# Kernel optimization log

Measured on AMD Instinct MI355X. Metric: run time of the kernel, lower is better.

Reference implementation:

```python
import jax, jax.numpy as jnp
import numpy as np

N_NODES = 50000
N_EDGES = 500000
N_FEAT = 128
EMB_DIM = 1024
HIDDEN = 128
OUT_DIM = 10
VOCAB = 55049
N_GRAPHS = 64


def setup_inputs() -> dict:
    key = jax.random.key(0)
    ks = jax.random.split(key, 12)
    x = jax.random.normal(ks[0], (N_NODES, N_FEAT), dtype=jnp.float32)
    edge_weight = jax.random.uniform(ks[1], (N_EDGES,), dtype=jnp.float32)
    edge_index = jax.random.randint(ks[2], (2, N_EDGES), 0, N_NODES)
    batch = jnp.sort(jax.random.randint(ks[3], (N_NODES,), 0, N_GRAPHS))
    node_ids = jax.random.randint(ks[4], (N_NODES,), 0, VOCAB)
    emb_table = jax.random.normal(ks[5], (VOCAB, EMB_DIM), dtype=jnp.float32)
    d_in = N_FEAT + EMB_DIM
    W1 = jax.random.normal(ks[6], (d_in, HIDDEN), dtype=jnp.float32) / np.sqrt(d_in)
    b1 = jnp.zeros((HIDDEN,), dtype=jnp.float32)
    W2 = jax.random.normal(ks[7], (HIDDEN, HIDDEN), dtype=jnp.float32) / np.sqrt(HIDDEN)
    b2 = jnp.zeros((HIDDEN,), dtype=jnp.float32)
    fcW = jax.random.normal(ks[8], (HIDDEN, OUT_DIM), dtype=jnp.float32) / np.sqrt(HIDDEN)
    fcb = jnp.zeros((OUT_DIM,), dtype=jnp.float32)
    return dict(x=x, edge_weight=edge_weight, emb_table=emb_table, W1=W1, b1=b1,
                W2=W2, b2=b2, fcW=fcW, fcb=fcb,
                edge_index=edge_index, batch=batch, node_ids=node_ids)


def gcn_conv(x, edge_index, edge_weight, W, b, n_nodes):
    # PyG GCNConv: x' = D^{-1/2} (A + I) D^{-1/2} (x W) + b, self-loop weight = 1
    x = x @ W
    src, dst = edge_index[0], edge_index[1]
    loop = jnp.arange(n_nodes)
    src = jnp.concatenate([src, loop])
    dst = jnp.concatenate([dst, loop])
    ew = jnp.concatenate([edge_weight, jnp.ones((n_nodes,), x.dtype)])
    deg = jax.ops.segment_sum(ew, dst, num_segments=n_nodes)
    dinv = jnp.where(deg > 0, jax.lax.rsqrt(deg), 0.0)
    norm = dinv[src] * ew * dinv[dst]  # [E+N]
    msgs = norm[:, None] * x[src]      # [E+N, H] gather
    out = jax.ops.segment_sum(msgs, dst, num_segments=n_nodes)  # scatter-add
    return out + b


def reference(x, edge_weight, emb_table, W1, b1, W2, b2, fcW, fcb,
              edge_index, batch, node_ids):
    n = x.shape[0]
    h = jnp.concatenate([x, emb_table[node_ids]], axis=1)  # [N, F+E]
    h = jax.nn.relu(gcn_conv(h, edge_index, edge_weight, W1, b1, n))
    h = jax.nn.relu(gcn_conv(h, edge_index, edge_weight, W2, b2, n))
    # global mean pool per graph (dropout is identity in eval)
    sums = jax.ops.segment_sum(h, batch, num_segments=N_GRAPHS)
    counts = jax.ops.segment_sum(jnp.ones((n,), h.dtype), batch, num_segments=N_GRAPHS)
    pooled = sums / jnp.maximum(counts, 1.0)[:, None]
    return pooled @ fcW + fcb
```

## Files before the change

### kernel.cpp

```cpp
#include <hip/hip_runtime.h>
#include <hip/hip_bf16.h>

#define N_NODES 50000
#define N_EDGES 500000
#define N_FEAT 128
#define EMB_DIM 1024
#define HIDDEN 128
#define OUT_DIM 10
#define N_GRAPHS 64
#define NB_NODE 196

typedef __attribute__((ext_vector_type(8))) short short8;
typedef __attribute__((ext_vector_type(4))) float f32x4;

__device__ __forceinline__ unsigned short f2bf(float f) {
    unsigned int u = __float_as_uint(f);
    return (unsigned short)((u + 0x7fffu + ((u >> 16) & 1u)) >> 16);
}
__device__ __forceinline__ float bflo(unsigned int r) { return __uint_as_float(r << 16); }
__device__ __forceinline__ float bfhi(unsigned int r) { return __uint_as_float(r & 0xffff0000u); }
__device__ __forceinline__ unsigned int packbf(float lo, float hi) {
    return ((unsigned int)f2bf(hi) << 16) | f2bf(lo);
}

__global__ __launch_bounds__(256) void k_init(unsigned long long* __restrict__ dc,
                                              float* __restrict__ sums,
                                              float* __restrict__ counts) {
    int i = blockIdx.x * 256 + threadIdx.x;
    if (i < N_NODES) dc[i] = 0ULL;
    if (i < N_GRAPHS * HIDDEN) sums[i] = 0.0f;
    if (i < N_GRAPHS) counts[i] = 0.0f;
}

__global__ __launch_bounds__(256) void k_deg(const int* __restrict__ dst,
                                             const float* __restrict__ ew,
                                             unsigned long long* __restrict__ dc) {
    int e = blockIdx.x * 256 + threadIdx.x;
    if (e < N_EDGES) {
        unsigned int fx = (unsigned int)(ew[e] * 16777216.0f);
        atomicAdd(&dc[dst[e]], (1ULL << 32) | (unsigned long long)fx);
    }
}

__global__ __launch_bounds__(256) void k_scan1(const unsigned long long* __restrict__ dc,
                                               int* __restrict__ bsum) {
    __shared__ int wsum[4];
    int i = blockIdx.x * 256 + threadIdx.x;
    int v = (i < N_NODES) ? (int)((const uint2*)dc)[i].y : 0;
#pragma unroll
    for (int off = 32; off; off >>= 1) v += __shfl_down(v, off, 64);
    if ((threadIdx.x & 63) == 0) wsum[threadIdx.x >> 6] = v;
    __syncthreads();
    if (threadIdx.x == 0) bsum[blockIdx.x] = wsum[0] + wsum[1] + wsum[2] + wsum[3];
}

__global__ __launch_bounds__(256) void k_scan2(int* __restrict__ bsum) {
    __shared__ int sh[256];
    int t = threadIdx.x;
    int v = (t < NB_NODE) ? bsum[t] : 0;
    sh[t] = v;
    __syncthreads();
    for (int off = 1; off < 256; off <<= 1) {
        int add = (t >= off) ? sh[t - off] : 0;
        __syncthreads();
        sh[t] += add;
        __syncthreads();
    }
    if (t < NB_NODE) bsum[t] = sh[t] - v;
}

__global__ __launch_bounds__(256) void k_scan3(const unsigned long long* __restrict__ dc,
                                               const int* __restrict__ bofs,
                                               int* __restrict__ cursor,
                                               int* __restrict__ rowptr,
                                               float* __restrict__ dinv) {
    __shared__ int sh[256];
    const int t = threadIdx.x;
    const int i = blockIdx.x * 256 + t;
    uint2 d = (i < N_NODES) ? ((const uint2*)dc)[i] : make_uint2(0u, 0u);
    int v = (int)d.y;
    sh[t] = v;
    __syncthreads();
    for (int off = 1; off < 256; off <<= 1) {
        int add = (t >= off) ? sh[t - off] : 0;
        __syncthreads();
        sh[t] += add;
        __syncthreads();
    }
    int ex = sh[t] - v + bofs[blockIdx.x];
    if (i < N_NODES) {
        rowptr[i] = ex;
        cursor[i] = ex;
        float deg = 1.0f + (float)d.x * (1.0f / 16777216.0f);
        dinv[i] = 1.0f / sqrtf(deg);
    }
    if (i == 0) rowptr[N_NODES] = N_EDGES;
}

__global__ __launch_bounds__(256) void k_fill(const int* __restrict__ src,
                                              const int* __restrict__ dst,
                                              const float* __restrict__ ew,
                                              const float* __restrict__ dinv,
                                              int* __restrict__ cursor,
                                              int2* __restrict__ csr) {
    int e = blockIdx.x * 256 + threadIdx.x;
    if (e >= N_EDGES) return;
    int s = src[e], d = dst[e];
    int pos = atomicAdd(&cursor[d], 1);
    float norm = dinv[s] * ew[e] * dinv[d];
    csr[pos] = make_int2(s, __float_as_int(norm));
}

__device__ __forceinline__ void prep_one(const float* __restrict__ W,
                                         unsigned short* __restrict__ Wt,
                                         int K, int t) {
    int n = t & 127;
    int c = t >> 7;
    if (c * 16 >= K) return;
    short8 h0, h1;
#pragma unroll
    for (int i = 0; i < 16; i++) {
        unsigned short h = f2bf(W[(size_t)(c * 16 + i) * HIDDEN + n]);
        if (i < 8) h0[i] = (short)h;
        else       h1[i - 8] = (short)h;
    }
    size_t o = (size_t)n * K + c * 16;
    *(short8*)&Wt[o] = h0;
    *(short8*)&Wt[o + 8] = h1;
}

__global__ __launch_bounds__(256) void k_prep(const float* __restrict__ W1,
                                              unsigned short* __restrict__ Wt1,
                                              const float* __restrict__ W2,
                                              unsigned short* __restrict__ Wt2) {
    int b = blockIdx.x;
    if (b < 36) prep_one(W1, Wt1, N_FEAT + EMB_DIM, b * 256 + threadIdx.x);
    else        prep_one(W2, Wt2, HIDDEN, (b - 36) * 256 + threadIdx.x);
}

template <int MODE>
__global__ __launch_bounds__(256) void k_gemm(const float* __restrict__ X,
                                              const unsigned short* __restrict__ Xb,
                                              const float* __restrict__ EMB,
                                              const int* __restrict__ ids,
                                              const unsigned short* __restrict__ Wt,
                                              unsigned short* __restrict__ tbf, int K) {
    __shared__ unsigned short As[128][40];
    __shared__ unsigned short Bs[128][40];

    const int tid = threadIdx.x;
    const int lane = tid & 63;
    const int wv = tid >> 6;
    const int wm = wv >> 1, wn = wv & 1;
    const int fr = lane & 15;
    const int fq = lane >> 4;
    const int mBase = blockIdx.x * 128;

    const int aRow = tid >> 1;
    const int aOff = (tid & 1) * 16;
    const int m = mBase + aRow;
    const int mc = (m < N_NODES) ? m : (N_NODES - 1);
    int embRow = 0;
    if (MODE == 0) embRow = ids[mc];

    f32x4 acc[4][4];
#pragma unroll
    for (int i = 0; i < 4; i++)
#pragma unroll
        for (int j = 0; j < 4; j++) acc[i][j] = (f32x4){0.f, 0.f, 0.f, 0.f};

    float av[16];
    short8 axb0, axb1;
    short8 bh0, bh1;
    {
        if (MODE == 0) {
            const float* aptr = X + (size_t)mc * N_FEAT + aOff;
            *(float4*)&av[0]  = *(const float4*)(aptr);
            *(float4*)&av[4]  = *(const float4*)(aptr + 4);
            *(float4*)&av[8]  = *(const float4*)(aptr + 8);
            *(float4*)&av[12] = *(const float4*)(aptr + 12);
        } else {
            const unsigned short* aptr = Xb + (size_t)mc * HIDDEN + aOff;
            axb0 = *(const short8*)(aptr);
            axb1 = *(const short8*)(aptr + 8);
        }
        size_t bo = (size_t)aRow * K + aOff;
        bh0 = *(const short8*)&Wt[bo];
        bh1 = *(const short8*)&Wt[bo + 8];
    }

    for (int k0 = 0; k0 < K; k0 += 32) {
        short8 ah0, ah1;
        if (MODE == 0) {
#pragma unroll
            for (int i = 0; i < 16; i++) {
                unsigned short h = f2bf(av[i]);
                if (i < 8) ah0[i] = (short)h;
                else       ah1[i - 8] = (short)h;
            }
        } else {
            ah0 = axb0; ah1 = axb1;
        }
        *(short8*)&As[aRow][aOff] = ah0; *(short8*)&As[aRow][aOff + 8] = ah1;
        *(short8*)&Bs[aRow][aOff] = bh0; *(short8*)&Bs[aRow][aOff + 8] = bh1;
        __syncthreads();

        int k1 = k0 + 32;
        if (k1 < K) {
            if (MODE == 0) {
                const float* aptr = (k1 < N_FEAT)
                    ? X + (size_t)mc * N_FEAT + k1 + aOff
                    : EMB + (size_t)embRow * EMB_DIM + (k1 - N_FEAT) + aOff;
                *(float4*)&av[0]  = *(const float4*)(aptr);
                *(float4*)&av[4]  = *(const float4*)(aptr + 4);
                *(float4*)&av[8]  = *(const float4*)(aptr + 8);
                *(float4*)&av[12] = *(const float4*)(aptr + 12);
            } else {
                const unsigned short* aptr = Xb + (size_t)mc * HIDDEN + k1 + aOff;
                axb0 = *(const short8*)(aptr);
                axb1 = *(const short8*)(aptr + 8);
            }
            size_t bo = (size_t)aRow * K + k1 + aOff;
            bh0 = *(const short8*)&Wt[bo];
            bh1 = *(const short8*)&Wt[bo + 8];
        }

        short8 aF[4], bF[4];
#pragma unroll
        for (int i = 0; i < 4; i++) {
            aF[i] = *(const short8*)&As[wm * 64 + i * 16 + fr][fq * 8];
            bF[i] = *(const short8*)&Bs[wn * 64 + i * 16 + fr][fq * 8];
        }

#pragma unroll
        for (int i = 0; i < 4; i++)
#pragma unroll
            for (int j = 0; j < 4; j++)
                acc[i][j] = __builtin_amdgcn_mfma_f32_16x16x32_bf16(aF[i], bF[j], acc[i][j], 0, 0, 0);
        __syncthreads();
    }

#pragma unroll
    for (int i = 0; i < 4; i++) {
#pragma unroll
        for (int j = 0; j < 4; j++) {
            int gcol = wn * 64 + j * 16 + fr;
#pragma unroll
            for (int r = 0; r < 4; r++) {
                int grow = mBase + wm * 64 + i * 16 + fq * 4 + r;
                if (grow < N_NODES) tbf[(size_t)grow * HIDDEN + gcol] = f2bf(acc[i][j][r]);
            }
        }
    }
}

template <int POOL, int NWAVE>
__global__ __launch_bounds__(NWAVE * 64) void k_agg(const int2* __restrict__ csr,
                                                    const int* __restrict__ rowptr,
                                                    const float* __restrict__ dinv,
                                                    const unsigned short* __restrict__ tbf,
                                                    const float* __restrict__ bias,
                                                    const int* __restrict__ batch,
                                                    unsigned short* __restrict__ outb,
                                                    float* __restrict__ sums,
                                                    float* __restrict__ counts) {
    __shared__ float lsum[HIDDEN];
    __shared__ int lcnt;
    const int wv = threadIdx.x >> 6;
    const int lane = threadIdx.x & 63;
    const int grp = lane >> 4;
    const int q = lane & 15;
    const int n = blockIdx.x * NWAVE + wv;
    const uint4* t128 = (const uint4*)tbf;

    if (POOL) {
        if (threadIdx.x < HIDDEN) lsum[threadIdx.x] = 0.f;
        if (threadIdx.x == 0) lcnt = 0;
        __syncthreads();
    }

    float acc[8] = {};
    if (n < N_NODES) {
        const int beg = rowptr[n];
        const int end = rowptr[n + 1];
        const float di = dinv[n];
        const float wself = (grp == 0) ? di * di : 0.f;
        uint4 sr = t128[(size_t)n * 16 + q];
        acc[0] = wself * bflo(sr.x); acc[1] = wself * bfhi(sr.x);
        acc[2] = wself * bflo(sr.y); acc[3] = wself * bfhi(sr.y);
        acc[4] = wself * bflo(sr.z); acc[5] = wself * bfhi(sr.z);
        acc[6] = wself * bflo(sr.w); acc[7] = wself * bfhi(sr.w);
        if (grp == 0) {
            float4 b0 = ((const float4*)bias)[q * 2];
            float4 b1 = ((const float4*)bias)[q * 2 + 1];
            acc[0] += b0.x; acc[1] += b0.y; acc[2] += b0.z; acc[3] += b0.w;
            acc[4] += b1.x; acc[5] += b1.y; acc[6] += b1.z; acc[7] += b1.w;
        }

        for (int base = beg; base < end; base += 64) {
            int cnt = end - base; if (cnt > 64) cnt = 64;
            int2 ce = (lane < cnt) ? csr[base + lane] : make_int2(0, 0);
            int j = 0;
            for (; j + 8 <= cnt; j += 8) {
                int   sA = __shfl(ce.x, j + grp);
                float wA = __int_as_float(__shfl(ce.y, j + grp));
                int   sB = __shfl(ce.x, j + 4 + grp);
                float wB = __int_as_float(__shfl(ce.y, j + 4 + grp));
                uint4 rA = t128[(size_t)sA * 16 + q];
                uint4 rB = t128[(size_t)sB * 16 + q];
                acc[0] = fmaf(wA, bflo(rA.x), acc[0]); acc[1] = fmaf(wA, bfhi(rA.x), acc[1]);
                acc[2] = fmaf(wA, bflo(rA.y), acc[2]); acc[3] = fmaf(wA, bfhi(rA.y), acc[3]);
                acc[4] = fmaf(wA, bflo(rA.z), acc[4]); acc[5] = fmaf(wA, bfhi(rA.z), acc[5]);
                acc[6] = fmaf(wA, bflo(rA.w), acc[6]); acc[7] = fmaf(wA, bfhi(rA.w), acc[7]);
                acc[0] = fmaf(wB, bflo(rB.x), acc[0]); acc[1] = fmaf(wB, bfhi(rB.x), acc[1]);
                acc[2] = fmaf(wB, bflo(rB.y), acc[2]); acc[3] = fmaf(wB, bfhi(rB.y), acc[3]);
                acc[4] = fmaf(wB, bflo(rB.z), acc[4]); acc[5] = fmaf(wB, bfhi(rB.z), acc[5]);
                acc[6] = fmaf(wB, bflo(rB.w), acc[6]); acc[7] = fmaf(wB, bfhi(rB.w), acc[7]);
            }
            for (; j < cnt; j += 4) {
                int   s = __shfl(ce.x, j + grp);
                float w = __int_as_float(__shfl(ce.y, j + grp));
                uint4 r = t128[(size_t)s * 16 + q];
                acc[0] = fmaf(w, bflo(r.x), acc[0]); acc[1] = fmaf(w, bfhi(r.x), acc[1]);
                acc[2] = fmaf(w, bflo(r.y), acc[2]); acc[3] = fmaf(w, bfhi(r.y), acc[3]);
                acc[4] = fmaf(w, bflo(r.z), acc[4]); acc[5] = fmaf(w, bfhi(r.z), acc[5]);
                acc[6] = fmaf(w, bflo(r.w), acc[6]); acc[7] = fmaf(w, bfhi(r.w), acc[7]);
            }
        }
    }

#pragma unroll
    for (int i = 0; i < 8; i++) {
        acc[i] += __shfl_xor(acc[i], 16);
        acc[i] += __shfl_xor(acc[i], 32);
    }

    if (!POOL) {
        if (n < N_NODES && grp == 0) {
#pragma unroll
            for (int i = 0; i < 8; i++) acc[i] = fmaxf(acc[i], 0.f);
            uint4 o;
            o.x = packbf(acc[0], acc[1]);
            o.y = packbf(acc[2], acc[3]);
            o.z = packbf(acc[4], acc[5]);
            o.w = packbf(acc[6], acc[7]);
            ((uint4*)outb)[(size_t)n * 16 + q] = o;
        }
    } else {
        if (n < N_NODES && grp == 0) {
#pragma unroll
            for (int i = 0; i < 8; i++) acc[i] = fmaxf(acc[i], 0.f);
            int g = batch[n];
            int g0 = batch[blockIdx.x * NWAVE];
            if (g == g0) {
#pragma unroll
                for (int i = 0; i < 8; i++) atomicAdd(&lsum[q * 8 + i], acc[i]);
                if (lane == 0) atomicAdd(&lcnt, 1);
            } else {
#pragma unroll
                for (int i = 0; i < 8; i++) atomicAdd(&sums[g * HIDDEN + q * 8 + i], acc[i]);
                if (lane == 0) atomicAdd(&counts[g], 1.0f);
            }
        }
        __syncthreads();
        int g0 = batch[blockIdx.x * NWAVE];
        if (threadIdx.x < HIDDEN) atomicAdd(&sums[g0 * HIDDEN + threadIdx.x], lsum[threadIdx.x]);
        if (threadIdx.x == 0) atomicAdd(&counts[g0], (float)lcnt);
    }
}

__global__ __launch_bounds__(64) void k_final(const float* __restrict__ sums,
                                              const float* __restrict__ counts,
                                              const float* __restrict__ fcW,
                                              const float* __restrict__ fcb,
                                              float* __restrict__ out) {
    int g = blockIdx.x;
    int o = threadIdx.x;
    if (o >= OUT_DIM) return;
    float inv = 1.0f / fmaxf(counts[g], 1.0f);
    float acc = 0.f;
    for (int f = 0; f < HIDDEN; f++)
        acc = fmaf(sums[g * HIDDEN + f], fcW[f * OUT_DIM + o], acc);
    out[g * OUT_DIM + o] = acc * inv + fcb[o];
}

extern "C" void kernel_launch(void* const* d_in, const int* in_sizes, int n_in,
                              void* d_out, int out_size, void* d_ws, size_t ws_size,
                              hipStream_t stream) {
    const float* x      = (const float*)d_in[0];
    const float* ew     = (const float*)d_in[1];
    const float* emb    = (const float*)d_in[2];
    const float* W1     = (const float*)d_in[3];
    const float* b1     = (const float*)d_in[4];
    const float* W2     = (const float*)d_in[5];
    const float* b2     = (const float*)d_in[6];
    const float* fcW    = (const float*)d_in[7];
    const float* fcb    = (const float*)d_in[8];
    const int* edge_idx = (const int*)d_in[9];
    const int* batch    = (const int*)d_in[10];
    const int* node_ids = (const int*)d_in[11];
    float* out = (float*)d_out;

    const int* src = edge_idx;
    const int* dst = edge_idx + N_EDGES;

    float* ws     = (float*)d_ws;
    float* dinv   = ws;
    unsigned long long* dc = (unsigned long long*)(ws + 50048);
    int*   cursor = (int*)(ws + 150048);
    int*   rowptr = (int*)(ws + 200096);
    int*   bsum   = (int*)(ws + 250152);
    int2*  csr    = (int2*)(ws + 250408);
    unsigned short* tbf   = (unsigned short*)(ws + 1250408);
    unsigned short* out1b = (unsigned short*)(ws + 4450408);
    float* sums   = ws + 7650408;
    float* counts = sums + N_GRAPHS * HIDDEN;
    unsigned short* wt1 = (unsigned short*)(ws + 7658664);
    unsigned short* wt2 = (unsigned short*)(ws + 7732392);

    const int NB_EDGE = (N_EDGES + 255) / 256;
    const int NB_GEMM = (N_NODES + 127) / 128;
    const int K1 = N_FEAT + EMB_DIM;

    k_init <<<NB_NODE, 256, 0, stream>>>(dc, sums, counts);
    k_deg  <<<NB_EDGE, 256, 0, stream>>>(dst, ew, dc);
    k_scan1<<<NB_NODE, 256, 0, stream>>>(dc, bsum);
    k_scan2<<<1, 256, 0, stream>>>(bsum);
    k_scan3<<<NB_NODE, 256, 0, stream>>>(dc, bsum, cursor, rowptr, dinv);
    k_fill <<<NB_EDGE, 256, 0, stream>>>(src, dst, ew, dinv, cursor, csr);
    k_prep <<<40, 256, 0, stream>>>(W1, wt1, W2, wt2);

    k_gemm<0><<<NB_GEMM, 256, 0, stream>>>(x, nullptr, emb, node_ids, wt1, tbf, K1);
    k_agg<0, 4><<<(N_NODES + 3) / 4, 256, 0, stream>>>(csr, rowptr, dinv, tbf, b1,
                                                       batch, out1b, sums, counts);

    k_gemm<1><<<NB_GEMM, 256, 0, stream>>>(nullptr, out1b, nullptr, nullptr, wt2, tbf, HIDDEN);
    k_agg<1, 16><<<(N_NODES + 15) / 16, 1024, 0, stream>>>(csr, rowptr, dinv, tbf, b2,
                                                           batch, nullptr, sums, counts);

    k_final<<<N_GRAPHS, 64, 0, stream>>>(sums, counts, fcW, fcb, out);
}
```

Baseline: 531.5 us.

## Map one node per 16-lane group in aggregation instead of one per wave

The GCN aggregation kernel now gives each 16-lane group its own destination node, so a wave handles four nodes rather than splitting one node's edges across four groups. This removes the cross-group shuffle reduction and the epilogue where three quarters of the lanes sat idle. Each group walks its edges in chunks of 16 with four gathers in flight, padding with zero-weight self entries. The second aggregation switches from 1024-thread blocks to 256-thread blocks. The cost is divergence inside a wave when the four nodes have different degrees.

After: 508.1 us. 4.4% less time.

```diff
diff --git a/kernel.cpp b/kernel.cpp
--- a/kernel.cpp
+++ b/kernel.cpp
@@ -270,7 +270,8 @@
     const int lane = threadIdx.x & 63;
     const int grp = lane >> 4;
     const int q = lane & 15;
-    const int n = blockIdx.x * NWAVE + wv;
+    const int gl = grp << 4;
+    const int n = (blockIdx.x * NWAVE + wv) * 4 + grp;
     const uint4* t128 = (const uint4*)tbf;
 
     if (POOL) {
@@ -284,59 +285,53 @@
         const int beg = rowptr[n];
         const int end = rowptr[n + 1];
         const float di = dinv[n];
-        const float wself = (grp == 0) ? di * di : 0.f;
+        const float wself = di * di;
         uint4 sr = t128[(size_t)n * 16 + q];
-        acc[0] = wself * bflo(sr.x); acc[1] = wself * bfhi(sr.x);
-        acc[2] = wself * bflo(sr.y); acc[3] = wself * bfhi(sr.y);
-        acc[4] = wself * bflo(sr.z); acc[5] = wself * bfhi(sr.z);
-        acc[6] = wself * bflo(sr.w); acc[7] = wself * bfhi(sr.w);
-        if (grp == 0) {
-            float4 b0 = ((const float4*)bias)[q * 2];
-            float4 b1 = ((const float4*)bias)[q * 2 + 1];
-            acc[0] += b0.x; acc[1] += b0.y; acc[2] += b0.z; acc[3] += b0.w;
-            acc[4] += b1.x; acc[5] += b1.y; acc[6] += b1.z; acc[7] += b1.w;
-        }
-
-        for (int base = beg; base < end; base += 64) {
-            int cnt = end - base; if (cnt > 64) cnt = 64;
-            int2 ce = (lane < cnt) ? csr[base + lane] : make_int2(0, 0);
-            int j = 0;
-            for (; j + 8 <= cnt; j += 8) {
-                int   sA = __shfl(ce.x, j + grp);
-                float wA = __int_as_float(__shfl(ce.y, j + grp));
-                int   sB = __shfl(ce.x, j + 4 + grp);
-                float wB = __int_as_float(__shfl(ce.y, j + 4 + grp));
-                uint4 rA = t128[(size_t)sA * 16 + q];
-                uint4 rB = t128[(size_t)sB * 16 + q];
-                acc[0] = fmaf(wA, bflo(rA.x), acc[0]); acc[1] = fmaf(wA, bfhi(rA.x), acc[1]);
-                acc[2] = fmaf(wA, bflo(rA.y), acc[2]); acc[3] = fmaf(wA, bfhi(rA.y), acc[3]);
-                acc[4] = fmaf(wA, bflo(rA.z), acc[4]); acc[5] = fmaf(wA, bfhi(rA.z), acc[5]);
-                acc[6] = fmaf(wA, bflo(rA.w), acc[6]); acc[7] = fmaf(wA, bfhi(rA.w), acc[7]);
-                acc[0] = fmaf(wB, bflo(rB.x), acc[0]); acc[1] = fmaf(wB, bfhi(rB.x), acc[1]);
-                acc[2] = fmaf(wB, bflo(rB.y), acc[2]); acc[3] = fmaf(wB, bfhi(rB.y), acc[3]);
-                acc[4] = fmaf(wB, bflo(rB.z), acc[4]); acc[5] = fmaf(wB, bfhi(rB.z), acc[5]);
-                acc[6] = fmaf(wB, bflo(rB.w), acc[6]); acc[7] = fmaf(wB, bfhi(rB.w), acc[7]);
+        float4 b0 = ((const float4*)bias)[q * 2];
+        float4 b1 = ((const float4*)bias)[q * 2 + 1];
+        acc[0] = fmaf(wself, bflo(sr.x), b0.x); acc[1] = fmaf(wself, bfhi(sr.x), b0.y);
+        acc[2] = fmaf(wself, bflo(sr.y), b0.z); acc[3] = fmaf(wself, bfhi(sr.y), b0.w);
+        acc[4] = fmaf(wself, bflo(sr.z), b1.x); acc[5] = fmaf(wself, bfhi(sr.z), b1.y);
+        acc[6] = fmaf(wself, bflo(sr.w), b1.z); acc[7] = fmaf(wself, bfhi(sr.w), b1.w);
+
+        for (int base = beg; base < end; base += 16) {
+            int cnt = end - base; if (cnt > 16) cnt = 16;
+            int2 ce = (q < cnt) ? csr[base + q] : make_int2(n, 0);
+            for (int j = 0; j < cnt; j += 4) {
+                int   s0 = __shfl(ce.x, gl + j);
+                float w0 = __int_as_float(__shfl(ce.y, gl + j));
+                int   s1 = __shfl(ce.x, gl + j + 1);
+                float w1 = __int_as_float(__shfl(ce.y, gl + j + 1));
+                int   s2 = __shfl(ce.x, gl + j + 2);
+                float w2 = __int_as_float(__shfl(ce.y, gl + j + 2));
+                int   s3 = __shfl(ce.x, gl + j + 3);
+                float w3 = __int_as_float(__shfl(ce.y, gl + j + 3));
+                uint4 r0 = t128[(size_t)s0 * 16 + q];
+                uint4 r1 = t128[(size_t)s1 * 16 + q];
+                uint4 r2 = t128[(size_t)s2 * 16 + q];
+                uint4 r3 = t128[(size_t)s3 * 16 + q];
+                acc[0] = fmaf(w0, bflo(r0.x), acc[0]); acc[1] = fmaf(w0, bfhi(r0.x), acc[1]);
+                acc[2] = fmaf(w0, bflo(r0.y), acc[2]); acc[3] = fmaf(w0, bfhi(r0.y), acc[3]);
+                acc[4] = fmaf(w0, bflo(r0.z), acc[4]); acc[5] = fmaf(w0, bfhi(r0.z), acc[5]);
+                acc[6] = fmaf(w0, bflo(r0.w), acc[6]); acc[7] = fmaf(w0, bfhi(r0.w), acc[7]);
+                acc[0] = fmaf(w1, bflo(r1.x), acc[0]); acc[1] = fmaf(w1, bfhi(r1.x), acc[1]);
+                acc[2] = fmaf(w1, bflo(r1.y), acc[2]); acc[3] = fmaf(w1, bfhi(r1.y), acc[3]);
+                acc[4] = fmaf(w1, bflo(r1.z), acc[4]); acc[5] = fmaf(w1, bfhi(r1.z), acc[5]);
+                acc[6] = fmaf(w1, bflo(r1.w), acc[6]); acc[7] = fmaf(w1, bfhi(r1.w), acc[7]);
+                acc[0] = fmaf(w2, bflo(r2.x), acc[0]); acc[1] = fmaf(w2, bfhi(r2.x), acc[1]);
+                acc[2] = fmaf(w2, bflo(r2.y), acc[2]); acc[3] = fmaf(w2, bfhi(r2.y), acc[3]);
+                acc[4] = fmaf(w2, bflo(r2.z), acc[4]); acc[5] = fmaf(w2, bfhi(r2.z), acc[5]);
+                acc[6] = fmaf(w2, bflo(r2.w), acc[6]); acc[7] = fmaf(w2, bfhi(r2.w), acc[7]);
+                acc[0] = fmaf(w3, bflo(r3.x), acc[0]); acc[1] = fmaf(w3, bfhi(r3.x), acc[1]);
+                acc[2] = fmaf(w3, bflo(r3.y), acc[2]); acc[3] = fmaf(w3, bfhi(r3.y), acc[3]);
+                acc[4] = fmaf(w3, bflo(r3.z), acc[4]); acc[5] = fmaf(w3, bfhi(r3.z), acc[5]);
+                acc[6] = fmaf(w3, bflo(r3.w), acc[6]); acc[7] = fmaf(w3, bfhi(r3.w), acc[7]);
             }
-            for (; j < cnt; j += 4) {
-                int   s = __shfl(ce.x, j + grp);
-                float w = __int_as_float(__shfl(ce.y, j + grp));
-                uint4 r = t128[(size_t)s * 16 + q];
-                acc[0] = fmaf(w, bflo(r.x), acc[0]); acc[1] = fmaf(w, bfhi(r.x), acc[1]);
-                acc[2] = fmaf(w, bflo(r.y), acc[2]); acc[3] = fmaf(w, bfhi(r.y), acc[3]);
-                acc[4] = fmaf(w, bflo(r.z), acc[4]); acc[5] = fmaf(w, bfhi(r.z), acc[5]);
-                acc[6] = fmaf(w, bflo(r.w), acc[6]); acc[7] = fmaf(w, bfhi(r.w), acc[7]);
-            }
-        }
-    }
-
-#pragma unroll
-    for (int i = 0; i < 8; i++) {
-        acc[i] += __shfl_xor(acc[i], 16);
-        acc[i] += __shfl_xor(acc[i], 32);
+        }
     }
 
     if (!POOL) {
-        if (n < N_NODES && grp == 0) {
+        if (n < N_NODES) {
 #pragma unroll
             for (int i = 0; i < 8; i++) acc[i] = fmaxf(acc[i], 0.f);
             uint4 o;
@@ -347,23 +342,23 @@
             ((uint4*)outb)[(size_t)n * 16 + q] = o;
         }
     } else {
-        if (n < N_NODES && grp == 0) {
+        if (n < N_NODES) {
 #pragma unroll
             for (int i = 0; i < 8; i++) acc[i] = fmaxf(acc[i], 0.f);
             int g = batch[n];
-            int g0 = batch[blockIdx.x * NWAVE];
+            int g0 = batch[blockIdx.x * NWAVE * 4];
             if (g == g0) {
 #pragma unroll
                 for (int i = 0; i < 8; i++) atomicAdd(&lsum[q * 8 + i], acc[i]);
-                if (lane == 0) atomicAdd(&lcnt, 1);
+                if (q == 0) atomicAdd(&lcnt, 1);
             } else {
 #pragma unroll
                 for (int i = 0; i < 8; i++) atomicAdd(&sums[g * HIDDEN + q * 8 + i], acc[i]);
-                if (lane == 0) atomicAdd(&counts[g], 1.0f);
+                if (q == 0) atomicAdd(&counts[g], 1.0f);
             }
         }
         __syncthreads();
-        int g0 = batch[blockIdx.x * NWAVE];
+        int g0 = batch[blockIdx.x * NWAVE * 4];
         if (threadIdx.x < HIDDEN) atomicAdd(&sums[g0 * HIDDEN + threadIdx.x], lsum[threadIdx.x]);
         if (threadIdx.x == 0) atomicAdd(&counts[g0], (float)lcnt);
     }
@@ -420,6 +415,7 @@
 
     const int NB_EDGE = (N_EDGES + 255) / 256;
     const int NB_GEMM = (N_NODES + 127) / 128;
+    const int NB_AGG  = (N_NODES + 15) / 16;
     const int K1 = N_FEAT + EMB_DIM;
 
     k_init <<<NB_NODE, 256, 0, stream>>>(dc, sums, counts);
@@ -431,12 +427,12 @@
     k_prep <<<40, 256, 0, stream>>>(W1, wt1, W2, wt2);
 
     k_gemm<0><<<NB_GEMM, 256, 0, stream>>>(x, nullptr, emb, node_ids, wt1, tbf, K1);
-    k_agg<0, 4><<<(N_NODES + 3) / 4, 256, 0, stream>>>(csr, rowptr, dinv, tbf, b1,
-                                                       batch, out1b, sums, counts);
+    k_agg<0, 4><<<NB_AGG, 256, 0, stream>>>(csr, rowptr, dinv, tbf, b1,
+                                            batch, out1b, sums, counts);
 
     k_gemm<1><<<NB_GEMM, 256, 0, stream>>>(nullptr, out1b, nullptr, nullptr, wt2, tbf, HIDDEN);
-    k_agg<1, 16><<<(N_NODES + 15) / 16, 1024, 0, stream>>>(csr, rowptr, dinv, tbf, b2,
-                                                           batch, nullptr, sums, counts);
+    k_agg<1, 4><<<NB_AGG, 256, 0, stream>>>(csr, rowptr, dinv, tbf, b2,
+                                            batch, nullptr, sums, counts);
 
     k_final<<<N_GRAPHS, 64, 0, stream>>>(sums, counts, fcW, fcb, out);
 }
```
